# Kernel optimization log

Hardware: AMD Instinct MI355X
Metric: run time of the kernel (lower is better)

## Reference

```python
import jax, jax.numpy as jnp
import numpy as np

B, T = 16, 8192
L, RC, DC, SC, EC, E, NC = 16, 32, 32, 256, 256, 100, 256


def conv1d(x, w, b, dilation=1):
    # x: [B, Cin, T], w: [Cout, Cin, K], b: [Cout]
    y = jax.lax.conv_general_dilated(
        x, w, window_strides=(1,), padding='VALID',
        rhs_dilation=(dilation,), dimension_numbers=('NCH', 'OIH', 'NCH'))
    return y + b[None, :, None]


def setup_inputs() -> dict:
    key = jax.random.key(0)
    ks = jax.random.split(key, 32)
    n = lambda k, shp: (jax.random.normal(k, shp) * 0.1).astype(jnp.float32)
    return dict(
        tokens=jax.random.randint(ks[0], (B, T), 0, NC),
        emb=n(ks[1], (NC, E)),
        init_w=n(ks[2], (RC, E, 1)), init_b=n(ks[3], (RC,)),
        dil_w=n(ks[4], (L, DC, RC, 2)), dil_b=n(ks[5], (L, DC)),
        filt_w=n(ks[6], (L, DC, DC, 2)), filt_b=n(ks[7], (L, DC)),
        gate_w=n(ks[8], (L, DC, DC, 2)), gate_b=n(ks[9], (L, DC)),
        res_w=n(ks[10], (L, RC, DC, 1)), res_b=n(ks[11], (L, RC)),
        skip_w=n(ks[12], (L, SC, DC, 1)), skip_b=n(ks[13], (L, SC)),
        end1_w=n(ks[14], (EC, SC, 1)), end1_b=n(ks[15], (EC,)),
        end2_w=n(ks[16], (EC, EC, 1)), end2_b=n(ks[17], (EC,)),
        fc1_w=n(ks[18], (128, 256)), fc1_b=n(ks[19], (128,)),
        fc2_w=n(ks[20], (128, 128)), fc2_b=n(ks[21], (128,)),
        fc3_w=n(ks[22], (64, 128)), fc3_b=n(ks[23], (64,)),
        fc4_w=n(ks[24], (NC, 64)), fc4_b=n(ks[25], (NC,)),
    )


def reference(tokens, emb, init_w, init_b, dil_w, dil_b, filt_w, filt_b,
              gate_w, gate_b, res_w, res_b, skip_w, skip_b,
              end1_w, end1_b, end2_w, end2_b,
              fc1_w, fc1_b, fc2_w, fc2_b, fc3_w, fc3_b, fc4_w, fc4_b):
    x = emb[tokens]                     # [B, T, E]
    x = jnp.transpose(x, (0, 2, 1))     # [B, E, T]
    x = conv1d(x, init_w, init_b)       # [B, RC, T]
    skip = None
    for i in range(L):
        d = 2 ** (i % 4)                # dilation resets each block of 4 layers
        xp = jnp.pad(x, ((0, 0), (0, 0), (d + 1, 0)))        # left pad d+1
        residual = conv1d(xp, dil_w[i], dil_b[i], dilation=d)  # [B, DC, T+1]
        f = jnp.tanh(conv1d(residual, filt_w[i], filt_b[i]))   # [B, DC, T]
        g = jax.nn.sigmoid(conv1d(residual, gate_w[i], gate_b[i]))
        x = f * g
        skip = conv1d(x, skip_w[i], skip_b[i])   # overwritten each layer (source bug, kept faithful)
        x = conv1d(x, res_w[i], res_b[i]) + residual[:, :, :-1]
    h = jax.nn.relu(conv1d(jax.nn.relu(skip), end1_w, end1_b))
    h = conv1d(h, end2_w, end2_b)       # [B, EC, T]
    h = h[:, :, -1]                     # [B, 256] last timestep only
    h = jax.nn.relu(h @ fc1_w.T + fc1_b)
    h = jax.nn.relu(h @ fc2_w.T + fc2_b)
    h = jax.nn.relu(h @ fc3_w.T + fc3_b)
    out = h @ fc4_w.T + fc4_b           # [B, NC]
    return out
```

## Files before the change

### kernel.cpp

```cpp
#include <hip/hip_runtime.h>


#define BB 16
#define TT 8192
#define LL 16
#define W0 77
#define NT 256

typedef __attribute__((ext_vector_type(8)))  short short8;
typedef __attribute__((ext_vector_type(16))) float float16;

#define MFMA_B16(a, b, c) __builtin_amdgcn_mfma_f32_32x32x16_bf16(a, b, c, 0, 0, 0)

__device__ __forceinline__ short f2bs(float f) {
  union { float ff; unsigned u; } v; v.ff = f;
  unsigned u = v.u;
  return (short)((u + 0x7FFFu + ((u >> 16) & 1u)) >> 16);
}
__device__ __forceinline__ float b2f(short h) {
  union { unsigned u; float f; } v;
  v.u = ((unsigned)(unsigned short)h) << 16; return v.f;
}
__device__ __forceinline__ float fast_sigmoid(float x) {
  return 1.f / (1.f + __expf(-x));
}
__device__ __forceinline__ float fast_tanh(float x) {
  return 2.f / (1.f + __expf(-2.f * x)) - 1.f;
}

__device__ __forceinline__ void afrag2(const short* src, int row, int kh, short8* out) {
  out[0] = *(const short8*)&src[row * 32 + 8 * kh];
  out[1] = *(const short8*)&src[row * 32 + 16 + 8 * kh];
}

__device__ __forceinline__ void load_chunk(
    int li, int cid, float* pf,
    const float* dil_w, const float* filt_w, const float* gate_w, const float* res_w)
{
  int mat = cid >> 7;
  int h = (cid >> 6) & 1, ln = cid & 63;
  int n = ln & 31, k2 = ln >> 5;
  int base = (li * 32 + n) * 32 + 16 * h + 8 * k2;
  if (mat == 6) {
    const float* p = res_w + base;
    #pragma unroll
    for (int j = 0; j < 8; j++) pf[j] = p[j];
  } else {
    const float* w = (mat < 2) ? dil_w : (mat < 4) ? filt_w : gate_w;
    const float* p = w + base * 2 + (mat & 1);
    #pragma unroll
    for (int j = 0; j < 8; j++) pf[j] = p[2 * j];
  }
}

__global__ __launch_bounds__(NT, 1) void wavenet_kernel(
    const int* __restrict__ tokens,
    const float* __restrict__ emb,
    const float* __restrict__ init_w, const float* __restrict__ init_b,
    const float* __restrict__ dil_w,  const float* __restrict__ dil_b,
    const float* __restrict__ filt_w, const float* __restrict__ filt_b,
    const float* __restrict__ gate_w, const float* __restrict__ gate_b,
    const float* __restrict__ res_w,  const float* __restrict__ res_b,
    const float* __restrict__ skip_w, const float* __restrict__ skip_b,
    const float* __restrict__ end1_w, const float* __restrict__ end1_b,
    const float* __restrict__ end2_w, const float* __restrict__ end2_b,
    const float* __restrict__ fc1_w,  const float* __restrict__ fc1_b,
    const float* __restrict__ fc2_w,  const float* __restrict__ fc2_b,
    const float* __restrict__ fc3_w,  const float* __restrict__ fc3_b,
    const float* __restrict__ fc4_w,  const float* __restrict__ fc4_b,
    float* __restrict__ out)
{
  __shared__ __align__(16) short bfw[2][7168];
  __shared__ float bias2[2][128];
  __shared__ __align__(16) short xbuf[W0 * 32];
  __shared__ __align__(16) short pool[8624];
  __shared__ int tok[W0];
  __shared__ float vecA[256], vecB[256];

  short* rb = pool;
  short* xm = pool + 2432;

  const int tid  = threadIdx.x;
  const int lane = tid & 63;
  const int wv   = tid >> 6;
  const int m    = lane & 31;
  const int kh   = lane >> 5;
  const int b    = blockIdx.x;

  if (tid < W0) tok[tid] = tokens[b * TT + (TT - 1 - tid)];
  __syncthreads();

  for (int cid = tid; cid < 77 * 14; cid += NT) {
    int u = cid / 14, s = cid % 14;
    const float* er = emb + tok[u] * 100 + s * 8;
    short8 v;
    if (s < 12) {
      #pragma unroll
      for (int j = 0; j < 8; j++) v[j] = f2bs(er[j]);
    } else if (s == 12) {
      #pragma unroll
      for (int j = 0; j < 4; j++) v[j] = f2bs(er[j]);
      #pragma unroll
      for (int j = 4; j < 8; j++) v[j] = 0;
    } else {
      #pragma unroll
      for (int j = 0; j < 8; j++) v[j] = 0;
    }
    *(short8*)&pool[u * 112 + s * 8] = v;
  }
  for (int cid = tid; cid < 896; cid += NT) {
    float pf[8];
    load_chunk(0, cid, pf, dil_w, filt_w, gate_w, res_w);
    short8 v;
    #pragma unroll
    for (int j = 0; j < 8; j++) v[j] = f2bs(pf[j]);
    *(short8*)&bfw[0][cid * 8] = v;
  }
  if (tid < 128) {
    const float* bsrc = (tid < 32) ? dil_b : (tid < 64) ? filt_b : (tid < 96) ? gate_b : res_b;
    bias2[0][tid] = bsrc[tid & 31];
  }
  __syncthreads();

  if (wv == 0) {
    short8 bi[7];
    #pragma unroll
    for (int s = 0; s < 7; s++) {
      const float* p = init_w + m * 100 + s * 16 + kh * 8;
      short8 v;
      if (s < 6) {
        #pragma unroll
        for (int j = 0; j < 8; j++) v[j] = f2bs(p[j]);
      } else if (kh == 0) {
        #pragma unroll
        for (int j = 0; j < 4; j++) v[j] = f2bs(p[j]);
        #pragma unroll
        for (int j = 4; j < 8; j++) v[j] = 0;
      } else {
        #pragma unroll
        for (int j = 0; j < 8; j++) v[j] = 0;
      }
      bi[s] = v;
    }
    const float binit = init_b[m];
    #pragma unroll
    for (int t = 0; t < 3; t++) {
      int R = t * 32;
      int u = R + m; if (u > 76) u = 76;
      float16 acc;
      #pragma unroll
      for (int r = 0; r < 16; r++) acc[r] = binit;
      #pragma unroll
      for (int s = 0; s < 7; s++) {
        short8 a = *(const short8*)&pool[u * 112 + s * 16 + kh * 8];
        acc = MFMA_B16(a, bi[s], acc);
      }
      #pragma unroll
      for (int r = 0; r < 16; r++) {
        int row = (r & 3) + 8 * (r >> 2) + 4 * kh;
        int uu = R + row;
        if (uu < W0) xbuf[uu * 32 + m] = f2bs(acc[r]);
      }
    }
  }
  __syncthreads();

  int Win = W0;
  for (int i = 0; i < LL; i++) {
    const int d = 1 << (i & 3);
    const int Wout = Win - d - 1;
    const int T = (Wout + 32) >> 5;
    const short* bw = bfw[i & 1];
    const float* bs = bias2[i & 1];

    float pf[4][8];
    float pbias = 0.f;
    const int nch = (tid < 128) ? 4 : 3;
    if (i + 1 < LL) {
      #pragma unroll
      for (int q = 0; q < 4; q++) {
        if (q < nch)
          load_chunk(i + 1, tid + q * NT, pf[q], dil_w, filt_w, gate_w, res_w);
      }
      if (tid < 128) {
        const float* bsrc = (tid < 32) ? dil_b : (tid < 64) ? filt_b : (tid < 96) ? gate_b : res_b;
        pbias = bsrc[(i + 1) * 32 + (tid & 31)];
      }
    }

    short8 BW[5][2];
    if (wv < T) {
      const int R = wv * 32;
      short8 B0[2], B1[2];
      #pragma unroll
      for (int h = 0; h < 2; h++) {
        B0[h] = *(const short8*)&bw[((0 * 2 + h) * 64 + lane) * 8];
        B1[h] = *(const short8*)&bw[((1 * 2 + h) * 64 + lane) * 8];
      }
      #pragma unroll
      for (int mt = 0; mt < 5; mt++)
        #pragma unroll
        for (int h = 0; h < 2; h++)
          BW[mt][h] = *(const short8*)&bw[(((mt + 2) * 2 + h) * 64 + lane) * 8];
      int vra = R + m + d; if (vra > Win - 1) vra = Win - 1;
      int vrz = R + m;     if (vrz > Win - 1) vrz = Win - 1;
      short8 aA[2], aZ[2];
      afrag2(xbuf, vra, kh, aA);
      afrag2(xbuf, vrz, kh, aZ);
      float16 acc;
      const float bc = bs[m];
      #pragma unroll
      for (int r = 0; r < 16; r++) acc[r] = bc;
      acc = MFMA_B16(aA[0], B0[0], acc);
      acc = MFMA_B16(aA[1], B0[1], acc);
      acc = MFMA_B16(aZ[0], B1[0], acc);
      acc = MFMA_B16(aZ[1], B1[1], acc);
      #pragma unroll
      for (int r = 0; r < 16; r++) {
        int row = (r & 3) + 8 * (r >> 2) + 4 * kh;
        int vr = R + row;
        if (vr <= Wout) rb[vr * 32 + m] = f2bs(acc[r]);
      }
    }
    __syncthreads();

    if (wv < T) {
      const int R = wv * 32;
      int r1 = R + m + 1; if (r1 > Wout) r1 = Wout;
      int r0 = R + m;     if (r0 > Wout) r0 = Wout;
      short8 a1[2], a0[2];
      afrag2(rb, r1, kh, a1);
      afrag2(rb, r0, kh, a0);
      float16 accF, accG;
      const float bf = bs[32 + m], bg = bs[64 + m];
      #pragma unroll
      for (int r = 0; r < 16; r++) { accF[r] = bf; accG[r] = bg; }
      accF = MFMA_B16(a1[0], BW[0][0], accF);
      accF = MFMA_B16(a1[1], BW[0][1], accF);
      accF = MFMA_B16(a0[0], BW[1][0], accF);
      accF = MFMA_B16(a0[1], BW[1][1], accF);
      accG = MFMA_B16(a1[0], BW[2][0], accG);
      accG = MFMA_B16(a1[1], BW[2][1], accG);
      accG = MFMA_B16(a0[0], BW[3][0], accG);
      accG = MFMA_B16(a0[1], BW[3][1], accG);
      #pragma unroll
      for (int r = 0; r < 16; r++) {
        int row = (r & 3) + 8 * (r >> 2) + 4 * kh;
        int uf = R + row;
        if (uf < Wout)
          xm[uf * 32 + m] = f2bs(fast_tanh(accF[r]) * fast_sigmoid(accG[r]));
      }
      asm volatile("s_waitcnt lgkmcnt(0)" ::: "memory");

      int rx = R + m; if (rx > Wout - 1) rx = Wout - 1;
      short8 aX[2];
      afrag2(xm, rx, kh, aX);
      float16 accX;
      const float br = bs[96 + m];
      #pragma unroll
      for (int r = 0; r < 16; r++) {
        int row = (r & 3) + 8 * (r >> 2) + 4 * kh;
        int rr = R + row + 1; if (rr > Wout) rr = Wout;
        accX[r] = br + b2f(rb[rr * 32 + m]);
      }
      accX = MFMA_B16(aX[0], BW[4][0], accX);
      accX = MFMA_B16(aX[1], BW[4][1], accX);
      #pragma unroll
      for (int r = 0; r < 16; r++) {
        int row = (r & 3) + 8 * (r >> 2) + 4 * kh;
        int uf = R + row;
        if (uf < Wout) xbuf[uf * 32 + m] = f2bs(accX[r]);
      }
    }

    if (i + 1 < LL) {
      short* dst = bfw[(i + 1) & 1];
      #pragma unroll
      for (int q = 0; q < 4; q++) {
        if (q < nch) {
          short8 v;
          #pragma unroll
          for (int j = 0; j < 8; j++) v[j] = f2bs(pf[q][j]);
          *(short8*)&dst[(tid + q * NT) * 8] = v;
        }
      }
      if (tid < 128) bias2[(i + 1) & 1][tid] = pbias;
    }
    __syncthreads();
    Win = Wout;
  }

  {
    float acc = skip_b[15 * 256 + tid];
    const float* wr = skip_w + (15 * 256 + tid) * 32;
    #pragma unroll
    for (int k = 0; k < 32; k += 4) {
      float4 w = *(const float4*)&wr[k];
      acc += (w.x * b2f(xm[k]) + w.y * b2f(xm[k+1])) + (w.z * b2f(xm[k+2]) + w.w * b2f(xm[k+3]));
    }
    vecA[tid] = fmaxf(acc, 0.f);
  }
  __syncthreads();
  {
    const float* wr = end1_w + tid * 256;
    float a4[4] = {0.f, 0.f, 0.f, 0.f};
    #pragma unroll 4
    for (int k = 0; k < 256; k += 16) {
      #pragma unroll
      for (int q = 0; q < 4; q++) {
        float4 w = *(const float4*)&wr[k + 4 * q];
        a4[q] += (w.x * vecA[k+4*q] + w.y * vecA[k+4*q+1]) + (w.z * vecA[k+4*q+2] + w.w * vecA[k+4*q+3]);
      }
    }
    vecB[tid] = fmaxf(end1_b[tid] + (a4[0] + a4[1]) + (a4[2] + a4[3]), 0.f);
  }
  __syncthreads();
  float h2;
  {
    const float* wr = end2_w + tid * 256;
    float a4[4] = {0.f, 0.f, 0.f, 0.f};
    #pragma unroll 4
    for (int k = 0; k < 256; k += 16) {
      #pragma unroll
      for (int q = 0; q < 4; q++) {
        float4 w = *(const float4*)&wr[k + 4 * q];
        a4[q] += (w.x * vecB[k+4*q] + w.y * vecB[k+4*q+1]) + (w.z * vecB[k+4*q+2] + w.w * vecB[k+4*q+3]);
      }
    }
    h2 = end2_b[tid] + (a4[0] + a4[1]) + (a4[2] + a4[3]);
  }
  __syncthreads();
  vecA[tid] = h2;
  __syncthreads();
  if (tid < 128) {
    const float* wr = fc1_w + tid * 256;
    float a4[4] = {0.f, 0.f, 0.f, 0.f};
    #pragma unroll 4
    for (int k = 0; k < 256; k += 16) {
      #pragma unroll
      for (int q = 0; q < 4; q++) {
        float4 w = *(const float4*)&wr[k + 4 * q];
        a4[q] += (w.x * vecA[k+4*q] + w.y * vecA[k+4*q+1]) + (w.z * vecA[k+4*q+2] + w.w * vecA[k+4*q+3]);
      }
    }
    vecB[tid] = fmaxf(fc1_b[tid] + (a4[0] + a4[1]) + (a4[2] + a4[3]), 0.f);
  }
  __syncthreads();
  if (tid < 128) {
    const float* wr = fc2_w + tid * 128;
    float a4[4] = {0.f, 0.f, 0.f, 0.f};
    #pragma unroll 2
    for (int k = 0; k < 128; k += 16) {
      #pragma unroll
      for (int q = 0; q < 4; q++) {
        float4 w = *(const float4*)&wr[k + 4 * q];
        a4[q] += (w.x * vecB[k+4*q] + w.y * vecB[k+4*q+1]) + (w.z * vecB[k+4*q+2] + w.w * vecB[k+4*q+3]);
      }
    }
    vecA[tid] = fmaxf(fc2_b[tid] + (a4[0] + a4[1]) + (a4[2] + a4[3]), 0.f);
  }
  __syncthreads();
  if (tid < 64) {
    const float* wr = fc3_w + tid * 128;
    float a4[4] = {0.f, 0.f, 0.f, 0.f};
    #pragma unroll 2
    for (int k = 0; k < 128; k += 16) {
      #pragma unroll
      for (int q = 0; q < 4; q++) {
        float4 w = *(const float4*)&wr[k + 4 * q];
        a4[q] += (w.x * vecA[k+4*q] + w.y * vecA[k+4*q+1]) + (w.z * vecA[k+4*q+2] + w.w * vecA[k+4*q+3]);
      }
    }
    vecB[tid] = fmaxf(fc3_b[tid] + (a4[0] + a4[1]) + (a4[2] + a4[3]), 0.f);
  }
  __syncthreads();
  {
    const float* wr = fc4_w + tid * 64;
    float a4[4] = {0.f, 0.f, 0.f, 0.f};
    #pragma unroll
    for (int k = 0; k < 64; k += 16) {
      #pragma unroll
      for (int q = 0; q < 4; q++) {
        float4 w = *(const float4*)&wr[k + 4 * q];
        a4[q] += (w.x * vecB[k+4*q] + w.y * vecB[k+4*q+1]) + (w.z * vecB[k+4*q+2] + w.w * vecB[k+4*q+3]);
      }
    }
    out[b * 256 + tid] = fc4_b[tid] + (a4[0] + a4[1]) + (a4[2] + a4[3]);
  }
}

extern "C" void kernel_launch(void* const* d_in, const int* in_sizes, int n_in,
                              void* d_out, int out_size, void* d_ws, size_t ws_size,
                              hipStream_t stream) {
  wavenet_kernel<<<BB, NT, 0, stream>>>(
      (const int*)d_in[0],    (const float*)d_in[1],  (const float*)d_in[2],  (const float*)d_in[3],
      (const float*)d_in[4],  (const float*)d_in[5],  (const float*)d_in[6],  (const float*)d_in[7],
      (const float*)d_in[8],  (const float*)d_in[9],  (const float*)d_in[10], (const float*)d_in[11],
      (const float*)d_in[12], (const float*)d_in[13], (const float*)d_in[14], (const float*)d_in[15],
      (const float*)d_in[16], (const float*)d_in[17], (const float*)d_in[18], (const float*)d_in[19],
      (const float*)d_in[20], (const float*)d_in[21], (const float*)d_in[22], (const float*)d_in[23],
      (const float*)d_in[24], (const float*)d_in[25], (float*)d_out);
}
```

Before: 211.7 us.

## Specialize idle waves for weight prefetch, parallelize init conv, fuse gating math

Several independent tweaks land together. In late layers with few active time tiles (T<=2), the next layer's weights are prefetched and converted only by the idle waves, and the compute waves skip that work. When a single wave is active, the block barrier is replaced by an LDS wait. The init conv is split across three waves instead of one, and tanh*sigmoid is fused into one reciprocal of a product of exponentials. The tail MLP now reads its activation vector with float4 LDS loads. The cost is more code paths and higher register use for the 7-chunk prefetch buffers.

```diff
diff --git a/kernel.cpp b/kernel.cpp
--- a/kernel.cpp
+++ b/kernel.cpp
@@ -20,12 +20,6 @@
 __device__ __forceinline__ float b2f(short h) {
   union { unsigned u; float f; } v;
   v.u = ((unsigned)(unsigned short)h) << 16; return v.f;
-}
-__device__ __forceinline__ float fast_sigmoid(float x) {
-  return 1.f / (1.f + __expf(-x));
-}
-__device__ __forceinline__ float fast_tanh(float x) {
-  return 2.f / (1.f + __expf(-2.f * x)) - 1.f;
 }
 
 __device__ __forceinline__ void afrag2(const short* src, int row, int kh, short8* out) {
@@ -75,7 +69,7 @@
   __shared__ __align__(16) short xbuf[W0 * 32];
   __shared__ __align__(16) short pool[8624];
   __shared__ int tok[W0];
-  __shared__ float vecA[256], vecB[256];
+  __shared__ __align__(16) float vecA[256], vecB[256];
 
   short* rb = pool;
   short* xm = pool + 2432;
@@ -122,7 +116,7 @@
   }
   __syncthreads();
 
-  if (wv == 0) {
+  if (wv < 3) {
     short8 bi[7];
     #pragma unroll
     for (int s = 0; s < 7; s++) {
@@ -143,24 +137,21 @@
       bi[s] = v;
     }
     const float binit = init_b[m];
-    #pragma unroll
-    for (int t = 0; t < 3; t++) {
-      int R = t * 32;
-      int u = R + m; if (u > 76) u = 76;
-      float16 acc;
-      #pragma unroll
-      for (int r = 0; r < 16; r++) acc[r] = binit;
-      #pragma unroll
-      for (int s = 0; s < 7; s++) {
-        short8 a = *(const short8*)&pool[u * 112 + s * 16 + kh * 8];
-        acc = MFMA_B16(a, bi[s], acc);
-      }
-      #pragma unroll
-      for (int r = 0; r < 16; r++) {
-        int row = (r & 3) + 8 * (r >> 2) + 4 * kh;
-        int uu = R + row;
-        if (uu < W0) xbuf[uu * 32 + m] = f2bs(acc[r]);
-      }
+    const int R = wv * 32;
+    int u = R + m; if (u > 76) u = 76;
+    float16 acc;
+    #pragma unroll
+    for (int r = 0; r < 16; r++) acc[r] = binit;
+    #pragma unroll
+    for (int s = 0; s < 7; s++) {
+      short8 a = *(const short8*)&pool[u * 112 + s * 16 + kh * 8];
+      acc = MFMA_B16(a, bi[s], acc);
+    }
+    #pragma unroll
+    for (int r = 0; r < 16; r++) {
+      int row = (r & 3) + 8 * (r >> 2) + 4 * kh;
+      int uu = R + row;
+      if (uu < W0) xbuf[uu * 32 + m] = f2bs(acc[r]);
     }
   }
   __syncthreads();
@@ -173,18 +164,30 @@
     const short* bw = bfw[i & 1];
     const float* bs = bias2[i & 1];
 
-    float pf[4][8];
+    float pfo[4][8];
     float pbias = 0.f;
     const int nch = (tid < 128) ? 4 : 3;
-    if (i + 1 < LL) {
+    const bool oldpf = (T >= 3) && (i + 1 < LL);
+    if (oldpf) {
       #pragma unroll
       for (int q = 0; q < 4; q++) {
         if (q < nch)
-          load_chunk(i + 1, tid + q * NT, pf[q], dil_w, filt_w, gate_w, res_w);
+          load_chunk(i + 1, tid + q * NT, pfo[q], dil_w, filt_w, gate_w, res_w);
       }
       if (tid < 128) {
         const float* bsrc = (tid < 32) ? dil_b : (tid < 64) ? filt_b : (tid < 96) ? gate_b : res_b;
         pbias = bsrc[(i + 1) * 32 + (tid & 31)];
+      }
+    }
+    const bool newpf = (T <= 2) && (i + 1 < LL) && (wv >= T);
+    const int nP = NT - T * 64;
+    const int ptid = tid - T * 64;
+    float pfn[7][8];
+    if (newpf) {
+      #pragma unroll
+      for (int q = 0; q < 7; q++) {
+        int c = ptid + q * nP;
+        if (c < 896) load_chunk(i + 1, c, pfn[q], dil_w, filt_w, gate_w, res_w);
       }
     }
 
@@ -222,7 +225,11 @@
         if (vr <= Wout) rb[vr * 32 + m] = f2bs(acc[r]);
       }
     }
-    __syncthreads();
+    if (T >= 2) {
+      __syncthreads();
+    } else {
+      asm volatile("s_waitcnt lgkmcnt(0)" ::: "memory");
+    }
 
     if (wv < T) {
       const int R = wv * 32;
@@ -247,8 +254,12 @@
       for (int r = 0; r < 16; r++) {
         int row = (r & 3) + 8 * (r >> 2) + 4 * kh;
         int uf = R + row;
-        if (uf < Wout)
-          xm[uf * 32 + m] = f2bs(fast_tanh(accF[r]) * fast_sigmoid(accG[r]));
+        if (uf < Wout) {
+          float u = __expf(-2.f * accF[r]);
+          float v = __expf(-accG[r]);
+          float fg = (1.f - u) * __builtin_amdgcn_rcpf((1.f + u) * (1.f + v));
+          xm[uf * 32 + m] = f2bs(fg);
+        }
       }
       asm volatile("s_waitcnt lgkmcnt(0)" ::: "memory");
 
@@ -271,16 +282,32 @@
         int uf = R + row;
         if (uf < Wout) xbuf[uf * 32 + m] = f2bs(accX[r]);
       }
-    }
-
-    if (i + 1 < LL) {
+    } else if (newpf) {
+      short* dst = bfw[(i + 1) & 1];
+      #pragma unroll
+      for (int q = 0; q < 7; q++) {
+        int c = ptid + q * nP;
+        if (c < 896) {
+          short8 v;
+          #pragma unroll
+          for (int j = 0; j < 8; j++) v[j] = f2bs(pfn[q][j]);
+          *(short8*)&dst[c * 8] = v;
+        }
+      }
+      for (int t2 = ptid; t2 < 128; t2 += nP) {
+        const float* bsrc = (t2 < 32) ? dil_b : (t2 < 64) ? filt_b : (t2 < 96) ? gate_b : res_b;
+        bias2[(i + 1) & 1][t2] = bsrc[(i + 1) * 32 + (t2 & 31)];
+      }
+    }
+
+    if (oldpf) {
       short* dst = bfw[(i + 1) & 1];
       #pragma unroll
       for (int q = 0; q < 4; q++) {
         if (q < nch) {
           short8 v;
           #pragma unroll
-          for (int j = 0; j < 8; j++) v[j] = f2bs(pf[q][j]);
+          for (int j = 0; j < 8; j++) v[j] = f2bs(pfo[q][j]);
           *(short8*)&dst[(tid + q * NT) * 8] = v;
         }
       }
@@ -309,7 +336,8 @@
       #pragma unroll
       for (int q = 0; q < 4; q++) {
         float4 w = *(const float4*)&wr[k + 4 * q];
-        a4[q] += (w.x * vecA[k+4*q] + w.y * vecA[k+4*q+1]) + (w.z * vecA[k+4*q+2] + w.w * vecA[k+4*q+3]);
+        float4 a = *(const float4*)&vecA[k + 4 * q];
+        a4[q] += (w.x * a.x + w.y * a.y) + (w.z * a.z + w.w * a.w);
       }
     }
     vecB[tid] = fmaxf(end1_b[tid] + (a4[0] + a4[1]) + (a4[2] + a4[3]), 0.f);
@@ -324,7 +352,8 @@
       #pragma unroll
       for (int q = 0; q < 4; q++) {
         float4 w = *(const float4*)&wr[k + 4 * q];
-        a4[q] += (w.x * vecB[k+4*q] + w.y * vecB[k+4*q+1]) + (w.z * vecB[k+4*q+2] + w.w * vecB[k+4*q+3]);
+        float4 a = *(const float4*)&vecB[k + 4 * q];
+        a4[q] += (w.x * a.x + w.y * a.y) + (w.z * a.z + w.w * a.w);
       }
     }
     h2 = end2_b[tid] + (a4[0] + a4[1]) + (a4[2] + a4[3]);
@@ -340,7 +369,8 @@
       #pragma unroll
       for (int q = 0; q < 4; q++) {
         float4 w = *(const float4*)&wr[k + 4 * q];
-        a4[q] += (w.x * vecA[k+4*q] + w.y * vecA[k+4*q+1]) + (w.z * vecA[k+4*q+2] + w.w * vecA[k+4*q+3]);
+        float4 a = *(const float4*)&vecA[k + 4 * q];
+        a4[q] += (w.x * a.x + w.y * a.y) + (w.z * a.z + w.w * a.w);
       }
     }
     vecB[tid] = fmaxf(fc1_b[tid] + (a4[0] + a4[1]) + (a4[2] + a4[3]), 0.f);
@@ -354,7 +384,8 @@
       #pragma unroll
       for (int q = 0; q < 4; q++) {
         float4 w = *(const float4*)&wr[k + 4 * q];
-        a4[q] += (w.x * vecB[k+4*q] + w.y * vecB[k+4*q+1]) + (w.z * vecB[k+4*q+2] + w.w * vecB[k+4*q+3]);
+        float4 a = *(const float4*)&vecB[k + 4 * q];
+        a4[q] += (w.x * a.x + w.y * a.y) + (w.z * a.z + w.w * a.w);
       }
     }
     vecA[tid] = fmaxf(fc2_b[tid] + (a4[0] + a4[1]) + (a4[2] + a4[3]), 0.f);
@@ -368,7 +399,8 @@
       #pragma unroll
       for (int q = 0; q < 4; q++) {
         float4 w = *(const float4*)&wr[k + 4 * q];
-        a4[q] += (w.x * vecA[k+4*q] + w.y * vecA[k+4*q+1]) + (w.z * vecA[k+4*q+2] + w.w * vecA[k+4*q+3]);
+        float4 a = *(const float4*)&vecA[k + 4 * q];
+        a4[q] += (w.x * a.x + w.y * a.y) + (w.z * a.z + w.w * a.w);
       }
     }
     vecB[tid] = fmaxf(fc3_b[tid] + (a4[0] + a4[1]) + (a4[2] + a4[3]), 0.f);
@@ -382,7 +414,8 @@
       #pragma unroll
       for (int q = 0; q < 4; q++) {
         float4 w = *(const float4*)&wr[k + 4 * q];
-        a4[q] += (w.x * vecB[k+4*q] + w.y * vecB[k+4*q+1]) + (w.z * vecB[k+4*q+2] + w.w * vecB[k+4*q+3]);
+        float4 a = *(const float4*)&vecB[k + 4 * q];
+        a4[q] += (w.x * a.x + w.y * a.y) + (w.z * a.z + w.w * a.w);
       }
     }
     out[b * 256 + tid] = fc4_b[tid] + (a4[0] + a4[1]) + (a4[2] + a4[3]);
```

New measurement: 208.4 us. About the same (-1.6%).
